# Performance work log

Hardware: AMD Instinct MI355X
Metric: run time of the kernel (lower is better)

The kernel has to match this reference:

```python
import jax, jax.numpy as jnp
import numpy as np

N_HEADS = 6
N_KV_HEADS = 2
HEAD_DIM = 128
REPEATS = N_HEADS // N_KV_HEADS  # 3


def setup_inputs() -> dict:
    key = jax.random.key(0)
    ks = jax.random.split(key, 5)
    B, S, D = 2, 4096, 768
    std = 1.0 / np.sqrt(D)
    return {
        "x": jax.random.normal(ks[0], (B, S, D), dtype=jnp.float32),
        "wq": jax.random.normal(ks[1], (D, N_HEADS * HEAD_DIM), dtype=jnp.float32) * std,
        "wk": jax.random.normal(ks[2], (D, N_KV_HEADS * HEAD_DIM), dtype=jnp.float32) * std,
        "wv": jax.random.normal(ks[3], (D, N_KV_HEADS * HEAD_DIM), dtype=jnp.float32) * std,
        "wo": jax.random.normal(ks[4], (N_HEADS * HEAD_DIM, D), dtype=jnp.float32) * std,
    }


def reference(x, wq, wk, wv, wo):
    B, S, _ = x.shape
    # projections
    q = (x @ wq).reshape(B, S, N_HEADS, HEAD_DIM)
    k = (x @ wk).reshape(B, S, N_KV_HEADS, HEAD_DIM)
    v = (x @ wv).reshape(B, S, N_KV_HEADS, HEAD_DIM)
    # GQA: repeat kv heads (repeat_interleave along head axis)
    k = jnp.repeat(k, REPEATS, axis=2)  # [B,S,H,D]
    v = jnp.repeat(v, REPEATS, axis=2)
    scale = 1.0 / jnp.sqrt(jnp.asarray(HEAD_DIM, x.dtype))
    # full bidirectional attention, [B,H,S,S] scores
    attn = jnp.einsum("bqhd,bkhd->bhqk", q * scale, k)
    attn = jax.nn.softmax(attn, axis=-1)
    out = jnp.einsum("bhqk,bkhd->bqhd", attn, v).reshape(B, S, N_HEADS * HEAD_DIM)
    return out @ wo
```

## Files before the change

kernel.cpp:

```cpp
#include <hip/hip_runtime.h>


typedef __attribute__((ext_vector_type(8))) short bf16x8;
typedef __attribute__((ext_vector_type(4))) float floatx4;
typedef __attribute__((ext_vector_type(4))) unsigned short ushort4v;

#define MFMA16(a, b, c) __builtin_amdgcn_mfma_f32_16x16x32_bf16((a), (b), (c), 0, 0, 0)

#if __has_builtin(__builtin_amdgcn_exp2f)
#define EXP2F(x) __builtin_amdgcn_exp2f(x)
#else
#define EXP2F(x) exp2f(x)
#endif

#define GLOAD_LDS16(gptr, lptr)                                                   \
  __builtin_amdgcn_global_load_lds(                                               \
      (const __attribute__((address_space(1))) unsigned int*)(gptr),              \
      (__attribute__((address_space(3))) unsigned int*)(lptr), 16, 0, 0)

__device__ __forceinline__ unsigned short f2bf(float f) {
  unsigned int u = __builtin_bit_cast(unsigned int, f);
  u = u + 0x7FFFu + ((u >> 16) & 1u);
  return (unsigned short)(u >> 16);
}

__device__ __forceinline__ unsigned short f2bf_fast(float f) {
  unsigned int u = __builtin_bit_cast(unsigned int, f);
  return (unsigned short)((u + 0x8000u) >> 16);
}

__device__ __forceinline__ float bf2f(unsigned short v) {
  return __builtin_bit_cast(float, (unsigned int)v << 16);
}


__global__ __launch_bounds__(256) void k_cvt_x(const float* __restrict__ x,
                                               unsigned short* __restrict__ xb, int n) {
  int i = (blockIdx.x * 256 + threadIdx.x) * 4;
  if (i + 3 < n) {
    float4 v = *(const float4*)(x + i);
    xb[i + 0] = f2bf(v.x);
    xb[i + 1] = f2bf(v.y);
    xb[i + 2] = f2bf(v.z);
    xb[i + 3] = f2bf(v.w);
  }
}

__global__ __launch_bounds__(256) void k_cvt_w(const float* __restrict__ wq,
                                               const float* __restrict__ wk,
                                               const float* __restrict__ wv,
                                               const float* __restrict__ wo,
                                               unsigned short* __restrict__ wqkvT,
                                               unsigned short* __restrict__ woT) {
  __shared__ float T[64 * 65];
  const float QSCALE = 1.4426950408889634f * 0.08838834764831843f;
  const int kb = blockIdx.x, nb = blockIdx.y, tid = threadIdx.x;

  const float* src; int ld, col0; unsigned short* dst; int n0; float scale = 1.0f;
  if (nb < 12)      { src = wq; ld = 768; col0 = nb * 64;        dst = wqkvT; n0 = nb * 64; scale = QSCALE; }
  else if (nb < 16) { src = wk; ld = 256; col0 = (nb - 12) * 64; dst = wqkvT; n0 = nb * 64; }
  else if (nb < 20) { src = wv; ld = 256; col0 = (nb - 16) * 64; dst = wqkvT; n0 = nb * 64; }
  else              { src = wo; ld = 768; col0 = (nb - 20) * 64; dst = woT;   n0 = (nb - 20) * 64; }

  const int k0 = kb * 64;
  {
    int cc = tid & 63, kk0 = tid >> 6;
#pragma unroll
    for (int it = 0; it < 16; it++) {
      int kk = kk0 + it * 4;
      T[kk * 65 + cc] = src[(size_t)(k0 + kk) * ld + col0 + cc] * scale;
    }
  }
  __syncthreads();
  {
    int kk = tid & 63, nn0 = tid >> 6;
#pragma unroll
    for (int it = 0; it < 16; it++) {
      int nn = nn0 + it * 4;
      dst[(size_t)(n0 + nn) * 768 + k0 + kk] = f2bf(T[kk * 65 + nn]);
    }
  }
}


__device__ __forceinline__ void store_out(float* C, int i, float v) { C[i] = v; }
__device__ __forceinline__ void store_out(unsigned short* C, int i, float v) { C[i] = f2bf(v); }

template <typename OUT_T, bool SPLIT_V>
__global__ __launch_bounds__(256) void k_gemm(const unsigned short* __restrict__ A, int lda,
                                              const unsigned short* __restrict__ Bt, int ldb,
                                              OUT_T* __restrict__ C, int ldc, int K,
                                              unsigned short* __restrict__ vTout) {
  __shared__ __align__(16) unsigned short As0[128 * 32];
  __shared__ __align__(16) unsigned short As1[128 * 32];
  __shared__ __align__(16) unsigned short Bs0[128 * 32];
  __shared__ __align__(16) unsigned short Bs1[128 * 32];

  const int tid = threadIdx.x;
  const int wave = tid >> 6, lane = tid & 63;
  const int quad = lane >> 4, l16 = lane & 15;
  const int wm = (wave >> 1) * 64, wn = (wave & 1) * 64;
  const int m0 = blockIdx.y * 128, n0 = blockIdx.x * 128;

  floatx4 acc[4][4] = {};

  auto stage = [&](const unsigned short* G, int ld, int row0, int k0, unsigned short* S) {
#pragma unroll
    for (int it = 0; it < 2; it++) {
      int j = it * 256 + tid;
      int r = j >> 2, c = (j & 3) ^ (r & 3);
      GLOAD_LDS16((const char*)(G + (size_t)(row0 + r) * ld + k0 + c * 8), &S[j * 8]);
    }
  };

  const int xq = (quad ^ (l16 & 3)) * 8;
  auto compute = [&](const unsigned short* As, const unsigned short* Bs) {
    bf16x8 af[4], bfr[4];
#pragma unroll
    for (int mf = 0; mf < 4; mf++)
      af[mf] = *(const bf16x8*)(&As[(wm + mf * 16 + l16) * 32 + xq]);
#pragma unroll
    for (int nf = 0; nf < 4; nf++)
      bfr[nf] = *(const bf16x8*)(&Bs[(wn + nf * 16 + l16) * 32 + xq]);
#pragma unroll
    for (int mf = 0; mf < 4; mf++)
#pragma unroll
      for (int nf = 0; nf < 4; nf++)
        acc[mf][nf] = MFMA16(af[mf], bfr[nf], acc[mf][nf]);
  };

  stage(A, lda, m0, 0, As0);
  stage(Bt, ldb, n0, 0, Bs0);

  const int half = K >> 6;
#pragma unroll 1
  for (int i = 0; i < half; i++) {
    __syncthreads();
    stage(A, lda, m0, (2 * i + 1) * 32, As1);
    stage(Bt, ldb, n0, (2 * i + 1) * 32, Bs1);
    compute(As0, Bs0);
    __syncthreads();
    if (i < half - 1) {
      stage(A, lda, m0, (2 * i + 2) * 32, As0);
      stage(Bt, ldb, n0, (2 * i + 2) * 32, Bs0);
    }
    compute(As1, Bs1);
  }

#pragma unroll
  for (int mf = 0; mf < 4; mf++)
#pragma unroll
    for (int nf = 0; nf < 4; nf++) {
      int col = n0 + wn + nf * 16 + l16;
      if (SPLIT_V && col >= 1024) {
        int cc = col - 1024;
        int kvhh = cc >> 7, d = cc & 127;
        int row0 = m0 + wm + mf * 16 + quad * 4;
        int bb = row0 >> 12, s = row0 & 4095;
        ushort4v pv;
        pv.x = f2bf(acc[mf][nf][0]);
        pv.y = f2bf(acc[mf][nf][1]);
        pv.z = f2bf(acc[mf][nf][2]);
        pv.w = f2bf(acc[mf][nf][3]);
        *(ushort4v*)(&vTout[((size_t)((bb * 2 + kvhh) * 128) + d) * 4096 + s]) = pv;
      } else {
#pragma unroll
        for (int r = 0; r < 4; r++) {
          int row = m0 + wm + mf * 16 + quad * 4 + r;
          store_out(C, row * ldc + col, acc[mf][nf][r]);
        }
      }
    }
}


#define NSEG 4

#define KS_OFF(row, c) (((row) << 7) + ((((c) ^ ((row) & 7))) << 3))
#define VS_OFF(row, c) (((row) << 6) + ((((c) ^ ((row) & 7))) << 3))

__global__ __launch_bounds__(256) void k_attn(const unsigned short* __restrict__ qkv,
                                              const unsigned short* __restrict__ vT,
                                              unsigned short* __restrict__ Opart,
                                              float* __restrict__ lpart) {
  __shared__ __align__(16) unsigned short Ks[64 * 128];
  __shared__ __align__(16) unsigned short Vt[128 * 64];
  __shared__ __align__(16) unsigned short Ps[128 * 64];

  const int qt = blockIdx.x, h = blockIdx.y;
  const int seg = blockIdx.z >> 1, b = blockIdx.z & 1;
  const int kvh = h / 3;
  const int tid = threadIdx.x, w = tid >> 6, lane = tid & 63;
  const int quad = lane >> 4, l16 = lane & 15;

  const char* qbase = (const char*)(qkv + (size_t)(b * 4096) * 1280 + h * 128);
  const char* kbase = (const char*)(qkv + (size_t)(b * 4096) * 1280 + 768 + kvh * 128);
  const char* vtb   = (const char*)(vT + (size_t)((b * 2 + kvh) * 128) * 4096);

  bf16x8 qf[2][4];
  floatx4 acc[2][8] = {};
  float l_i[2] = {0.f, 0.f};

#pragma unroll
  for (int it = 0; it < 8; it++) {
    int cb = it * 256 + w * 64;
    int j = cb + lane;
    int r = j >> 4, c = (j & 15) ^ (r & 7);
    unsigned short* dst = (cb < 1024) ? &Ks[cb * 8] : &Vt[(cb - 1024) * 8];
    GLOAD_LDS16(qbase + (size_t)(qt * 128 + r) * 2560 + c * 16, dst);
  }
  __syncthreads();

  {
    const unsigned short* qsrc = (w < 2) ? Ks : Vt;
    const int qr0 = (w & 1) * 32;
#pragma unroll
    for (int qg = 0; qg < 2; qg++)
#pragma unroll
      for (int dc = 0; dc < 4; dc++)
        qf[qg][dc] = *(const bf16x8*)(&qsrc[KS_OFF(qr0 + qg * 16 + l16, dc * 4 + quad)]);
  }
  __syncthreads();

  auto stage_k = [&](int kt) {
#pragma unroll
    for (int it = 0; it < 4; it++) {
      int cb = it * 256 + w * 64;
      int j = cb + lane;
      int r = j >> 4, c = (j & 15) ^ (r & 7);
      GLOAD_LDS16(kbase + (size_t)(kt * 64 + r) * 2560 + c * 16, &Ks[cb * 8]);
    }
  };
  auto stage_v = [&](int kt) {
#pragma unroll
    for (int it = 0; it < 4; it++) {
      int cb = it * 256 + w * 64;
      int j = cb + lane;
      int r = j >> 3, c = (j & 7) ^ (r & 7);
      GLOAD_LDS16(vtb + (size_t)r * 8192 + kt * 128 + c * 16, &Vt[cb * 8]);
    }
  };

  const int k0 = seg * 16;
  stage_k(k0);

#pragma unroll 1
  for (int i = 0; i < 16; i++) {
    __syncthreads();
    stage_v(k0 + i);

#pragma unroll
    for (int nfh = 0; nfh < 2; nfh++) {
      floatx4 sfr[2][2] = {};
      __builtin_amdgcn_s_setprio(1);
#pragma unroll
      for (int nfo = 0; nfo < 2; nfo++) {
        int nf = nfh * 2 + nfo;
#pragma unroll
        for (int dc = 0; dc < 4; dc++) {
          bf16x8 kf = *(const bf16x8*)(&Ks[KS_OFF(nf * 16 + l16, dc * 4 + quad)]);
          sfr[0][nfo] = MFMA16(kf, qf[0][dc], sfr[0][nfo]);
          sfr[1][nfo] = MFMA16(kf, qf[1][dc], sfr[1][nfo]);
        }
      }
      __builtin_amdgcn_s_setprio(0);
#pragma unroll
      for (int qg = 0; qg < 2; qg++)
#pragma unroll
        for (int nfo = 0; nfo < 2; nfo++) {
          int nf = nfh * 2 + nfo;
          float p0 = EXP2F(sfr[qg][nfo][0]);
          float p1 = EXP2F(sfr[qg][nfo][1]);
          float p2 = EXP2F(sfr[qg][nfo][2]);
          float p3 = EXP2F(sfr[qg][nfo][3]);
          l_i[qg] += (p0 + p1) + (p2 + p3);
          int row = w * 32 + qg * 16 + l16;
          int ch = nf * 2 + (quad >> 1);
          ushort4v pw;
          pw.x = f2bf_fast(p0);
          pw.y = f2bf_fast(p1);
          pw.z = f2bf_fast(p2);
          pw.w = f2bf_fast(p3);
          *(ushort4v*)(&Ps[VS_OFF(row, ch) + (quad & 1) * 4]) = pw;
        }
    }

    __syncthreads();
    if (i < 15) stage_k(k0 + i + 1);

    __builtin_amdgcn_s_setprio(1);
#pragma unroll
    for (int kc = 0; kc < 2; kc++) {
      bf16x8 pf0 = *(const bf16x8*)(&Ps[VS_OFF(w * 32 + l16, kc * 4 + quad)]);
      bf16x8 pf1 = *(const bf16x8*)(&Ps[VS_OFF(w * 32 + 16 + l16, kc * 4 + quad)]);
#pragma unroll
      for (int df = 0; df < 8; df++) {
        bf16x8 vf = *(const bf16x8*)(&Vt[VS_OFF(df * 16 + l16, kc * 4 + quad)]);
        acc[0][df] = MFMA16(pf0, vf, acc[0][df]);
        acc[1][df] = MFMA16(pf1, vf, acc[1][df]);
      }
    }
    __builtin_amdgcn_s_setprio(0);
  }

#pragma unroll
  for (int qg = 0; qg < 2; qg++) {
    float lt = l_i[qg];
    lt += __shfl_xor(lt, 16, 64);
    lt += __shfl_xor(lt, 32, 64);
    if (quad == 0)
      lpart[((size_t)(seg * 2 + b) * 6 + h) * 4096 + qt * 128 + w * 32 + qg * 16 + l16] = lt;
#pragma unroll
    for (int r = 0; r < 4; r++) {
      int row = qt * 128 + w * 32 + qg * 16 + quad * 4 + r;
      unsigned short* orow =
          Opart + (size_t)seg * 8192 * 768 + (size_t)(b * 4096 + row) * 768 + h * 128;
#pragma unroll
      for (int df = 0; df < 8; df++)
        orow[df * 16 + l16] = f2bf_fast(acc[qg][df][r]);
    }
  }
}

__global__ __launch_bounds__(256) void k_reduce(const unsigned short* __restrict__ Opart,
                                                const float* __restrict__ lpart,
                                                unsigned short* __restrict__ ob) {
  int idx = (blockIdx.x * 256 + threadIdx.x) * 4;
  int row = idx / 768, col = idx - row * 768;
  int h = col >> 7;
  int b = row >> 12, r = row & 4095;

  float lt = 0.f;
#pragma unroll
  for (int s = 0; s < NSEG; s++)
    lt += lpart[((size_t)(s * 2 + b) * 6 + h) * 4096 + r];
  float inv = 1.0f / lt;

  float acc0 = 0.f, acc1 = 0.f, acc2 = 0.f, acc3 = 0.f;
#pragma unroll
  for (int s = 0; s < NSEG; s++) {
    ushort4v v = *(const ushort4v*)(&Opart[(size_t)s * 8192 * 768 + idx]);
    acc0 += bf2f(v.x);
    acc1 += bf2f(v.y);
    acc2 += bf2f(v.z);
    acc3 += bf2f(v.w);
  }
  ushort4v o;
  o.x = f2bf(acc0 * inv);
  o.y = f2bf(acc1 * inv);
  o.z = f2bf(acc2 * inv);
  o.w = f2bf(acc3 * inv);
  *(ushort4v*)(&ob[idx]) = o;
}


extern "C" void kernel_launch(void* const* d_in, const int* in_sizes, int n_in,
                              void* d_out, int out_size, void* d_ws, size_t ws_size,
                              hipStream_t stream) {
  const float* x  = (const float*)d_in[0];
  const float* wq = (const float*)d_in[1];
  const float* wk = (const float*)d_in[2];
  const float* wv = (const float*)d_in[3];
  const float* wo = (const float*)d_in[4];
  float* out = (float*)d_out;

  char* ws = (char*)d_ws;
  unsigned short* xb    = (unsigned short*)(ws);
  unsigned short* wqkvT = (unsigned short*)(ws + 12582912);
  unsigned short* woT   = (unsigned short*)(ws + 14548992);
  unsigned short* qkvb  = (unsigned short*)(ws + 15728640);
  unsigned short* ob    = (unsigned short*)(ws + 36700160);
  unsigned short* Opart = (unsigned short*)(ws + 49283072);
  float*          lpart = (float*)(ws + 99614720);
  unsigned short* vT    = ob;

  k_cvt_x<<<6144, 256, 0, stream>>>(x, xb, 8192 * 768);
  k_cvt_w<<<dim3(12, 32), 256, 0, stream>>>(wq, wk, wv, wo, wqkvT, woT);

  k_gemm<unsigned short, true><<<dim3(10, 64), 256, 0, stream>>>(
      xb, 768, wqkvT, 768, qkvb, 1280, 768, vT);

  k_attn<<<dim3(32, 6, 2 * NSEG), 256, 0, stream>>>(qkvb, vT, Opart, lpart);

  k_reduce<<<6144, 256, 0, stream>>>(Opart, lpart, ob);

  k_gemm<float, false><<<dim3(6, 64), 256, 0, stream>>>(ob, 768, woT, 768, out, 768, 768, nullptr);
}
```

Measured before the change: 256.5 us.

## Switch attention to 32x32 MFMA and keep P in registers via lane shuffles

Rewrites the attention inner loop to use 32x32x16 bf16 MFMA for both QK^T and PV, where it previously used 16x16x32 tiles. The score tile now lands in a layout that lets the softmax probabilities be packed to bf16 and exchanged across half-waves with shuffles, so the shared-memory P buffer and its store/load round trip are gone. This cuts LDS traffic and LDS footprint and lowers the instruction count per MFMA. In exchange it adds cross-lane shuffles and select logic, and the larger accumulators increase register pressure.

Result: slower. 268.3 us (+4.6%).

```diff
diff --git a/kernel.cpp b/kernel.cpp
--- a/kernel.cpp
+++ b/kernel.cpp
@@ -3,9 +3,12 @@
 
 typedef __attribute__((ext_vector_type(8))) short bf16x8;
 typedef __attribute__((ext_vector_type(4))) float floatx4;
+typedef __attribute__((ext_vector_type(16))) float floatx16;
 typedef __attribute__((ext_vector_type(4))) unsigned short ushort4v;
+typedef __attribute__((ext_vector_type(4))) unsigned int uint4v;
 
 #define MFMA16(a, b, c) __builtin_amdgcn_mfma_f32_16x16x32_bf16((a), (b), (c), 0, 0, 0)
+#define MFMA32(a, b, c) __builtin_amdgcn_mfma_f32_32x32x16_bf16((a), (b), (c), 0, 0, 0)
 
 #if __has_builtin(__builtin_amdgcn_exp2f)
 #define EXP2F(x) __builtin_amdgcn_exp2f(x)
@@ -31,6 +34,12 @@
 
 __device__ __forceinline__ float bf2f(unsigned short v) {
   return __builtin_bit_cast(float, (unsigned int)v << 16);
+}
+
+__device__ __forceinline__ unsigned int pack_bf16(float a, float b) {
+  unsigned int ua = __builtin_bit_cast(unsigned int, a);
+  unsigned int ub = __builtin_bit_cast(unsigned int, b);
+  return ((ua + 0x8000u) >> 16) | ((ub + 0x8000u) & 0xFFFF0000u);
 }
 
 
@@ -185,21 +194,20 @@
                                               float* __restrict__ lpart) {
   __shared__ __align__(16) unsigned short Ks[64 * 128];
   __shared__ __align__(16) unsigned short Vt[128 * 64];
-  __shared__ __align__(16) unsigned short Ps[128 * 64];
 
   const int qt = blockIdx.x, h = blockIdx.y;
   const int seg = blockIdx.z >> 1, b = blockIdx.z & 1;
   const int kvh = h / 3;
   const int tid = threadIdx.x, w = tid >> 6, lane = tid & 63;
-  const int quad = lane >> 4, l16 = lane & 15;
+  const int lo = lane & 31, hi = lane >> 5;
 
   const char* qbase = (const char*)(qkv + (size_t)(b * 4096) * 1280 + h * 128);
   const char* kbase = (const char*)(qkv + (size_t)(b * 4096) * 1280 + 768 + kvh * 128);
   const char* vtb   = (const char*)(vT + (size_t)((b * 2 + kvh) * 128) * 4096);
 
-  bf16x8 qf[2][4];
-  floatx4 acc[2][8] = {};
-  float l_i[2] = {0.f, 0.f};
+  bf16x8 qf[8];
+  floatx16 acc[4] = {};
+  float l_i = 0.f;
 
 #pragma unroll
   for (int it = 0; it < 8; it++) {
@@ -213,12 +221,10 @@
 
   {
     const unsigned short* qsrc = (w < 2) ? Ks : Vt;
-    const int qr0 = (w & 1) * 32;
-#pragma unroll
-    for (int qg = 0; qg < 2; qg++)
-#pragma unroll
-      for (int dc = 0; dc < 4; dc++)
-        qf[qg][dc] = *(const bf16x8*)(&qsrc[KS_OFF(qr0 + qg * 16 + l16, dc * 4 + quad)]);
+    const int qr = (w & 1) * 32 + lo;
+#pragma unroll
+    for (int dc = 0; dc < 8; dc++)
+      qf[dc] = *(const bf16x8*)(&qsrc[KS_OFF(qr, dc * 2 + hi)]);
   }
   __syncthreads();
 
@@ -249,77 +255,72 @@
     __syncthreads();
     stage_v(k0 + i);
 
-#pragma unroll
-    for (int nfh = 0; nfh < 2; nfh++) {
-      floatx4 sfr[2][2] = {};
-      __builtin_amdgcn_s_setprio(1);
-#pragma unroll
-      for (int nfo = 0; nfo < 2; nfo++) {
-        int nf = nfh * 2 + nfo;
-#pragma unroll
-        for (int dc = 0; dc < 4; dc++) {
-          bf16x8 kf = *(const bf16x8*)(&Ks[KS_OFF(nf * 16 + l16, dc * 4 + quad)]);
-          sfr[0][nfo] = MFMA16(kf, qf[0][dc], sfr[0][nfo]);
-          sfr[1][nfo] = MFMA16(kf, qf[1][dc], sfr[1][nfo]);
-        }
-      }
-      __builtin_amdgcn_s_setprio(0);
-#pragma unroll
-      for (int qg = 0; qg < 2; qg++)
-#pragma unroll
-        for (int nfo = 0; nfo < 2; nfo++) {
-          int nf = nfh * 2 + nfo;
-          float p0 = EXP2F(sfr[qg][nfo][0]);
-          float p1 = EXP2F(sfr[qg][nfo][1]);
-          float p2 = EXP2F(sfr[qg][nfo][2]);
-          float p3 = EXP2F(sfr[qg][nfo][3]);
-          l_i[qg] += (p0 + p1) + (p2 + p3);
-          int row = w * 32 + qg * 16 + l16;
-          int ch = nf * 2 + (quad >> 1);
-          ushort4v pw;
-          pw.x = f2bf_fast(p0);
-          pw.y = f2bf_fast(p1);
-          pw.z = f2bf_fast(p2);
-          pw.w = f2bf_fast(p3);
-          *(ushort4v*)(&Ps[VS_OFF(row, ch) + (quad & 1) * 4]) = pw;
-        }
-    }
+    floatx16 sfr[2] = {};
+    __builtin_amdgcn_s_setprio(1);
+#pragma unroll
+    for (int t = 0; t < 2; t++)
+#pragma unroll
+      for (int dc = 0; dc < 8; dc++) {
+        bf16x8 kf = *(const bf16x8*)(&Ks[KS_OFF(t * 32 + lo, dc * 2 + hi)]);
+        sfr[t] = MFMA32(kf, qf[dc], sfr[t]);
+      }
+    __builtin_amdgcn_s_setprio(0);
+
+    unsigned int pk[2][4][2];
+#pragma unroll
+    for (int t = 0; t < 2; t++)
+#pragma unroll
+      for (int rp = 0; rp < 4; rp++) {
+        float p0 = EXP2F(sfr[t][rp * 4 + 0]);
+        float p1 = EXP2F(sfr[t][rp * 4 + 1]);
+        float p2 = EXP2F(sfr[t][rp * 4 + 2]);
+        float p3 = EXP2F(sfr[t][rp * 4 + 3]);
+        l_i += (p0 + p1) + (p2 + p3);
+        pk[t][rp][0] = pack_bf16(p0, p1);
+        pk[t][rp][1] = pack_bf16(p2, p3);
+      }
 
     __syncthreads();
     if (i < 15) stage_k(k0 + i + 1);
 
     __builtin_amdgcn_s_setprio(1);
 #pragma unroll
-    for (int kc = 0; kc < 2; kc++) {
-      bf16x8 pf0 = *(const bf16x8*)(&Ps[VS_OFF(w * 32 + l16, kc * 4 + quad)]);
-      bf16x8 pf1 = *(const bf16x8*)(&Ps[VS_OFF(w * 32 + 16 + l16, kc * 4 + quad)]);
-#pragma unroll
-      for (int df = 0; df < 8; df++) {
-        bf16x8 vf = *(const bf16x8*)(&Vt[VS_OFF(df * 16 + l16, kc * 4 + quad)]);
-        acc[0][df] = MFMA16(pf0, vf, acc[0][df]);
-        acc[1][df] = MFMA16(pf1, vf, acc[1][df]);
+    for (int kc = 0; kc < 4; kc++) {
+      const int t = kc >> 1, rpA = (kc & 1) * 2;
+      unsigned int s0 = hi ? pk[t][rpA][0] : pk[t][rpA + 1][0];
+      unsigned int s1 = hi ? pk[t][rpA][1] : pk[t][rpA + 1][1];
+      unsigned int r0 = __shfl_xor(s0, 32, 64);
+      unsigned int r1 = __shfl_xor(s1, 32, 64);
+      uint4v fr;
+      fr[0] = hi ? r0 : pk[t][rpA][0];
+      fr[1] = hi ? r1 : pk[t][rpA][1];
+      fr[2] = hi ? pk[t][rpA + 1][0] : r0;
+      fr[3] = hi ? pk[t][rpA + 1][1] : r1;
+      bf16x8 pf = __builtin_bit_cast(bf16x8, fr);
+#pragma unroll
+      for (int dt = 0; dt < 4; dt++) {
+        bf16x8 vf = *(const bf16x8*)(&Vt[VS_OFF(dt * 32 + lo, kc * 2 + hi)]);
+        acc[dt] = MFMA32(pf, vf, acc[dt]);
       }
     }
     __builtin_amdgcn_s_setprio(0);
   }
 
-#pragma unroll
-  for (int qg = 0; qg < 2; qg++) {
-    float lt = l_i[qg];
-    lt += __shfl_xor(lt, 16, 64);
-    lt += __shfl_xor(lt, 32, 64);
-    if (quad == 0)
-      lpart[((size_t)(seg * 2 + b) * 6 + h) * 4096 + qt * 128 + w * 32 + qg * 16 + l16] = lt;
-#pragma unroll
-    for (int r = 0; r < 4; r++) {
-      int row = qt * 128 + w * 32 + qg * 16 + quad * 4 + r;
-      unsigned short* orow =
-          Opart + (size_t)seg * 8192 * 768 + (size_t)(b * 4096 + row) * 768 + h * 128;
-#pragma unroll
-      for (int df = 0; df < 8; df++)
-        orow[df * 16 + l16] = f2bf_fast(acc[qg][df][r]);
-    }
-  }
+  {
+    float lt = l_i + __shfl_xor(l_i, 32, 64);
+    if (hi == 0)
+      lpart[((size_t)(seg * 2 + b) * 6 + h) * 4096 + qt * 128 + w * 32 + lo] = lt;
+  }
+#pragma unroll
+  for (int dt = 0; dt < 4; dt++)
+#pragma unroll
+    for (int rp = 0; rp < 4; rp++)
+#pragma unroll
+      for (int j = 0; j < 4; j++) {
+        int row = qt * 128 + w * 32 + j + rp * 8 + hi * 4;
+        Opart[(size_t)seg * 8192 * 768 + (size_t)(b * 4096 + row) * 768 + h * 128 +
+              dt * 32 + lo] = f2bf_fast(acc[dt][rp * 4 + j]);
+      }
 }
 
 __global__ __launch_bounds__(256) void k_reduce(const unsigned short* __restrict__ Opart,
```
